# Kernel tuning notes

Measured on AMD Instinct MI355X. Metric: run time of the kernel, lower is better.

Reference implementation:

```python
import jax, jax.numpy as jnp
import numpy as np

DIM = 512
A_HEADS = 8
C_HEADS = 4
DH = 64
EPS = 1e-5


def layer_norm(x, g, b):
    mu = jnp.mean(x, axis=-1, keepdims=True)
    var = jnp.var(x, axis=-1, keepdims=True)
    return (x - mu) * jax.lax.rsqrt(var + EPS) * g + b


def setup_inputs() -> dict:
    key = jax.random.key(0)
    ks = jax.random.split(key, 8)
    inner_a = A_HEADS * DH  # 512
    inner_c = C_HEADS * DH  # 256
    s = 0.02
    return {
        "x": jax.random.normal(ks[0], (4, 192, DIM), dtype=jnp.float32),
        # Attention branch params
        "ln1_g": jnp.ones((DIM,), jnp.float32),
        "ln1_b": jnp.zeros((DIM,), jnp.float32),
        "Wqkv": jax.random.normal(ks[1], (DIM, 3 * inner_a), jnp.float32) * s,
        "Wo": jax.random.normal(ks[2], (inner_a, DIM), jnp.float32) * s,
        "bo": jnp.zeros((DIM,), jnp.float32),
        # Trittention branch params
        "ln2_g": jnp.ones((DIM,), jnp.float32),
        "ln2_b": jnp.zeros((DIM,), jnp.float32),
        "Wabcde": jax.random.normal(ks[3], (DIM, 5 * inner_c), jnp.float32) * s,
        "babcde": jnp.zeros((5 * inner_c,), jnp.float32),
        "Wp": jax.random.normal(ks[4], (inner_c, DIM), jnp.float32) * s,
        "bp": jnp.zeros((DIM,), jnp.float32),
    }


def _attention(x, ln_g, ln_b, Wqkv, Wo, bo):
    B, T, _ = x.shape
    xn = layer_norm(x, ln_g, ln_b)
    qkv = xn @ Wqkv  # [B,T,3*H*D]
    q, k, v = jnp.split(qkv, 3, axis=-1)
    def heads(t):
        return t.reshape(B, T, A_HEADS, DH).transpose(0, 2, 1, 3)  # [B,H,T,D]
    q, k, v = heads(q), heads(k), heads(v)
    scale = DH ** -0.5
    dots = jnp.einsum('bhqd,bhkd->bhqk', q, k) * scale
    attn = jax.nn.softmax(dots, axis=-1)
    out = jnp.einsum('bhqk,bhkd->bhqd', attn, v)
    out = out.transpose(0, 2, 1, 3).reshape(B, T, A_HEADS * DH)
    return out @ Wo + bo


def _trittention(x, ln_g, ln_b, Wabcde, babcde, Wp, bp):
    B, T, _ = x.shape
    xn = layer_norm(x, ln_g, ln_b)
    proj = xn @ Wabcde + babcde  # [B,T,5*H*D]
    a, b_, c, d_, e = jnp.split(proj, 5, axis=-1)
    def heads(t):
        return t.reshape(B, T, C_HEADS, DH)  # [B,T,H,D]
    a, b_, c, d_, e = heads(a), heads(b_), heads(c), heads(d_), heads(e)
    # cubic score: [B,H,S,T,Q]
    score = jnp.einsum('bshd,bthd,bqhd->bhstq', a, b_, c) / DH
    # softmax over joint (s,t) for each query q
    score = score.transpose(0, 1, 4, 2, 3).reshape(B, C_HEADS, T, T * T)
    attn = jax.nn.softmax(score, axis=-1).reshape(B, C_HEADS, T, T, T)
    z = (jnp.einsum('bhqst,bshd->bhqd', attn, d_)
         + jnp.einsum('bhqst,bthd->bhqd', attn, e))
    z = z.transpose(0, 2, 1, 3).reshape(B, T, C_HEADS * DH)
    return z @ Wp + bp


def reference(x, ln1_g, ln1_b, Wqkv, Wo, bo, ln2_g, ln2_b, Wabcde, babcde, Wp, bp):
    return (_attention(x, ln1_g, ln1_b, Wqkv, Wo, bo)
            + _trittention(x, ln2_g, ln2_b, Wabcde, babcde, Wp, bp))
```

## Files before the change

kernel.cpp:

```cpp
#include <hip/hip_runtime.h>
#include <cstdint>


#define B_   4
#define T_   192
#define DIM_ 512
#define AH   8
#define CH   4

typedef unsigned short u16;
typedef unsigned int   u32;
typedef __attribute__((ext_vector_type(8))) short short8;
typedef __attribute__((ext_vector_type(4))) float floatx4;
typedef __attribute__((ext_vector_type(4))) int intx4;
typedef __attribute__((ext_vector_type(2))) float f32x2;
typedef __attribute__((ext_vector_type(8))) _Float16 half8;
typedef __attribute__((ext_vector_type(2))) _Float16 half2v;
typedef __attribute__((ext_vector_type(2))) __fp16 fp16x2;

union Frag  { intx4 i; short8 s; };
union FragH { intx4 i; half8 h; };

__device__ __forceinline__ floatx4 mfma16(Frag a, Frag b, floatx4 c) {
    return __builtin_amdgcn_mfma_f32_16x16x32_bf16(a.s, b.s, c, 0, 0, 0);
}
__device__ __forceinline__ floatx4 mfma16h(FragH a, FragH b, floatx4 c) {
    return __builtin_amdgcn_mfma_f32_16x16x32_f16(a.h, b.h, c, 0, 0, 0);
}

__device__ __forceinline__ float fexp2(float x) {
    return __builtin_amdgcn_exp2f(x);
}

__device__ __forceinline__ float wave_reduce_sum(float v) {
#pragma unroll
    for (int off = 32; off >= 1; off >>= 1)
        v += __shfl_xor(v, off, 64);
    return v;
}

__device__ __forceinline__ u32 pack_rne(float x, float y) {
    u32 ux = __float_as_uint(x);
    u32 uy = __float_as_uint(y);
    ux += 0x7fffu + ((ux >> 16) & 1u);
    uy += 0x7fffu + ((uy >> 16) & 1u);
    return (ux >> 16) | (uy & 0xffff0000u);
}
__device__ __forceinline__ u16 bf16_rne(float x) {
    u32 u = __float_as_uint(x);
    u += 0x7fffu + ((u >> 16) & 1u);
    return (u16)(u >> 16);
}
__device__ __forceinline__ float bf16f(u16 h) { return __uint_as_float(((u32)h) << 16); }

__device__ __forceinline__ u32 pack_f16(float x, float y) {
    union { fp16x2 h; u32 u; } cv;
    cv.h = __builtin_amdgcn_cvt_pkrtz(x, y);
    return cv.u;
}
__device__ __forceinline__ u32 mul_h2(u32 a, u32 b) {
    union { u32 u; half2v h; } ua, ub, uw;
    ua.u = a; ub.u = b;
    uw.h = ua.h * ub.h;
    return uw.u;
}

__device__ __forceinline__ Frag ld_frag8(const u16* p) {
    Frag f;
    uint2 a = *(const uint2*)p;
    uint2 b = *(const uint2*)(p + 4);
    f.i = (intx4){ (int)a.x, (int)a.y, (int)b.x, (int)b.y };
    return f;
}

#define LOG2E 1.44269504088896f

__global__ __launch_bounds__(256) void prep_kernel(
    const float* __restrict__ x,
    const float* __restrict__ g1, const float* __restrict__ b1,
    const float* __restrict__ g2, const float* __restrict__ b2,
    u16* __restrict__ x1h, u16* __restrict__ x2h,
    const float* __restrict__ Wqkv, u16* __restrict__ wqh,
    const float* __restrict__ Wab,  u16* __restrict__ wah,
    const float* __restrict__ Wo,   const float* __restrict__ Wp,
    u16* __restrict__ wofh)
{
    __shared__ union { float t[64][65]; float red[4][2]; } u;
    const int tid = threadIdx.x;
    if (blockIdx.x < 768) {
        int row = blockIdx.x;
        const float2 v = ((const float2*)(x + (size_t)row * DIM_))[tid];
        float s  = v.x + v.y;
        float s2 = v.x * v.x + v.y * v.y;
        s  = wave_reduce_sum(s);
        s2 = wave_reduce_sum(s2);
        int w = tid >> 6;
        if ((tid & 63) == 0) { u.red[w][0] = s; u.red[w][1] = s2; }
        __syncthreads();
        float ts  = u.red[0][0] + u.red[1][0] + u.red[2][0] + u.red[3][0];
        float ts2 = u.red[0][1] + u.red[1][1] + u.red[2][1] + u.red[3][1];
        float mean = ts * (1.0f / DIM_);
        float var  = ts2 * (1.0f / DIM_) - mean * mean;
        float rstd = rsqrtf(var + 1e-5f);
        int c0 = tid * 2;
        float n0 = (v.x - mean) * rstd;
        float n1 = (v.y - mean) * rstd;
        float a0 = n0 * g1[c0] + b1[c0], a1 = n1 * g1[c0 + 1] + b1[c0 + 1];
        float c2 = n0 * g2[c0] + b2[c0], c3 = n1 * g2[c0 + 1] + b2[c0 + 1];
        size_t o = (size_t)row * 256 + tid;
        ((u32*)x1h)[o] = pack_rne(a0, a1);
        ((u32*)x2h)[o] = pack_rne(c2, c3);
        return;
    }
    int id = blockIdx.x - 768;
    const float* W; u16 *H; int K, N, Kout, kofs, tile;
    if (id < 192)      { W = Wqkv; H = wqh;  K = 512; N = 1536; Kout = 512; kofs = 0;   tile = id;       }
    else if (id < 352) { W = Wab;  H = wah;  K = 512; N = 1280; Kout = 512; kofs = 0;   tile = id - 192; }
    else if (id < 416) { W = Wo;   H = wofh; K = 512; N = 512;  Kout = 768; kofs = 0;   tile = id - 352; }
    else               { W = Wp;   H = wofh; K = 256; N = 512;  Kout = 768; kofs = 512; tile = id - 416; }
    int nx = N >> 6;
    int n0 = (tile % nx) * 64, k0 = (tile / nx) * 64;
    int rr = tid >> 4, c4 = (tid & 15) << 2;
#pragma unroll
    for (int p = 0; p < 4; ++p) {
        int row = rr + p * 16;
        float4 v = *(const float4*)(W + (size_t)(k0 + row) * N + n0 + c4);
        u.t[row][c4 + 0] = v.x; u.t[row][c4 + 1] = v.y;
        u.t[row][c4 + 2] = v.z; u.t[row][c4 + 3] = v.w;
    }
    __syncthreads();
#pragma unroll
    for (int p = 0; p < 4; ++p) {
        int n = rr + p * 16;
        u16 hi[4];
#pragma unroll
        for (int c = 0; c < 4; ++c)
            hi[c] = bf16_rne(u.t[c4 + c][n]);
        size_t o = (size_t)(n0 + n) * Kout + kofs + k0 + c4;
        *(uint2*)&H[o] = make_uint2((u32)hi[0] | ((u32)hi[1] << 16), (u32)hi[2] | ((u32)hi[3] << 16));
    }
}

__global__ __launch_bounds__(256) void gemm_dual(
    const u16* __restrict__ x1h, const u16* __restrict__ wqh,
    const u16* __restrict__ x2h, const u16* __restrict__ wah,
    const float* __restrict__ babcde,
    float* __restrict__ qkv, float* __restrict__ proj)
{
    __shared__ u16 As[64][68];
    __shared__ u16 Bs[64][68];
    const int tid = threadIdx.x;
    const int nb = blockIdx.x;
    const u16 *Ah, *BTh; const float* bias; float* C; int N, bn;
    if (nb < 24) { Ah = x1h; BTh = wqh; bias = nullptr; C = qkv;  N = 1536; bn = nb * 64; }
    else         { Ah = x2h; BTh = wah; bias = babcde; C = proj; N = 1280; bn = (nb - 24) * 64; }
    const int K = 512;
    const int bm = blockIdx.y * 64;
    const int lane = tid & 63, wave = tid >> 6;
    const int m16 = lane & 15, quad = lane >> 4;
    const int wm = (wave >> 1) * 32, wn = (wave & 1) * 32;
    const int r = tid >> 2, c16 = (tid & 3) * 16;

    floatx4 acc[2][2];
#pragma unroll
    for (int i = 0; i < 2; ++i)
#pragma unroll
        for (int j = 0; j < 2; ++j) acc[i][j] = (floatx4){0.f, 0.f, 0.f, 0.f};

    for (int k0 = 0; k0 < K; k0 += 64) {
        __syncthreads();
        {
            const u16* pa = Ah + (size_t)(bm + r) * K + k0 + c16;
            uint4 v0 = *(const uint4*)pa, v1 = *(const uint4*)(pa + 8);
            *(uint2*)&As[r][c16 + 0]  = make_uint2(v0.x, v0.y);
            *(uint2*)&As[r][c16 + 4]  = make_uint2(v0.z, v0.w);
            *(uint2*)&As[r][c16 + 8]  = make_uint2(v1.x, v1.y);
            *(uint2*)&As[r][c16 + 12] = make_uint2(v1.z, v1.w);
        }
        {
            const u16* pb = BTh + (size_t)(bn + r) * K + k0 + c16;
            uint4 v0 = *(const uint4*)pb, v1 = *(const uint4*)(pb + 8);
            *(uint2*)&Bs[r][c16 + 0]  = make_uint2(v0.x, v0.y);
            *(uint2*)&Bs[r][c16 + 4]  = make_uint2(v0.z, v0.w);
            *(uint2*)&Bs[r][c16 + 8]  = make_uint2(v1.x, v1.y);
            *(uint2*)&Bs[r][c16 + 12] = make_uint2(v1.z, v1.w);
        }
        __syncthreads();
#pragma unroll
        for (int ks = 0; ks < 2; ++ks) {
            const int ko = ks * 32 + quad * 8;
            Frag a0 = ld_frag8(&As[wm + m16][ko]);
            Frag a1 = ld_frag8(&As[wm + 16 + m16][ko]);
            Frag b0 = ld_frag8(&Bs[wn + m16][ko]);
            Frag b1 = ld_frag8(&Bs[wn + 16 + m16][ko]);
            acc[0][0] = mfma16(a0, b0, acc[0][0]);
            acc[0][1] = mfma16(a0, b1, acc[0][1]);
            acc[1][0] = mfma16(a1, b0, acc[1][0]);
            acc[1][1] = mfma16(a1, b1, acc[1][1]);
        }
    }
#pragma unroll
    for (int i = 0; i < 2; ++i)
#pragma unroll
        for (int rr = 0; rr < 4; ++rr) {
            int m = bm + wm + i * 16 + quad * 4 + rr;
#pragma unroll
            for (int j = 0; j < 2; ++j) {
                int n = bn + wn + j * 16 + m16;
                float v = acc[i][j][rr];
                if (bias) v += bias[n];
                C[(size_t)m * N + n] = v;
            }
        }
}

__global__ __launch_bounds__(256) void gemm_epilogue(
    const u16* __restrict__ aoh, const u16* __restrict__ zh,
    const u16* __restrict__ BTh,
    const float* __restrict__ bo, const float* __restrict__ bp,
    float* __restrict__ C)
{
    __shared__ u16 As[32][68];
    __shared__ u16 Bs[64][68];
    const int tid = threadIdx.x;
    const int bm = blockIdx.y * 32, bn = blockIdx.x * 64;
    const int lane = tid & 63, wave = tid >> 6;
    const int m16 = lane & 15, quad = lane >> 4;
    const int wm = (wave >> 1) * 16, wn = (wave & 1) * 32;
    const int ra = tid >> 3, c8 = (tid & 7) * 8;
    const int rb = tid >> 2, c16 = (tid & 3) * 16;
    const int N = 512, K = 768;

    floatx4 acc[2];
    acc[0] = (floatx4){0.f, 0.f, 0.f, 0.f};
    acc[1] = (floatx4){0.f, 0.f, 0.f, 0.f};

    for (int k0 = 0; k0 < K; k0 += 64) {
        __syncthreads();
        {
            const u16* pah = (k0 < 512)
                ? aoh + (size_t)(bm + ra) * 512 + k0 + c8
                : zh  + (size_t)(bm + ra) * 256 + (k0 - 512) + c8;
            uint4 v = *(const uint4*)pah;
            *(uint2*)&As[ra][c8 + 0] = make_uint2(v.x, v.y);
            *(uint2*)&As[ra][c8 + 4] = make_uint2(v.z, v.w);
        }
        {
            const u16* pb = BTh + (size_t)(bn + rb) * K + k0 + c16;
            uint4 v0 = *(const uint4*)pb, v1 = *(const uint4*)(pb + 8);
            *(uint2*)&Bs[rb][c16 + 0]  = make_uint2(v0.x, v0.y);
            *(uint2*)&Bs[rb][c16 + 4]  = make_uint2(v0.z, v0.w);
            *(uint2*)&Bs[rb][c16 + 8]  = make_uint2(v1.x, v1.y);
            *(uint2*)&Bs[rb][c16 + 12] = make_uint2(v1.z, v1.w);
        }
        __syncthreads();
#pragma unroll
        for (int ks = 0; ks < 2; ++ks) {
            const int ko = ks * 32 + quad * 8;
            Frag ah = ld_frag8(&As[wm + m16][ko]);
            Frag b0 = ld_frag8(&Bs[wn + m16][ko]);
            Frag b1 = ld_frag8(&Bs[wn + 16 + m16][ko]);
            acc[0] = mfma16(ah, b0, acc[0]);
            acc[1] = mfma16(ah, b1, acc[1]);
        }
    }
#pragma unroll
    for (int rr = 0; rr < 4; ++rr) {
        int m = bm + wm + quad * 4 + rr;
#pragma unroll
        for (int j = 0; j < 2; ++j) {
            int n = bn + wn + j * 16 + m16;
            C[(size_t)m * N + n] = acc[j][rr] + bo[n] + bp[n];
        }
    }
}

__global__ __launch_bounds__(256) void attn_mfma(
    const float* __restrict__ qkv, u16* __restrict__ aoh)
{
    __shared__ union { u16 Ks[192][68]; u16 P[32][196]; } KP;
    __shared__ union { u16 Vt[64][196]; struct { float m[2][16][68]; float r[2][16]; } mg; } VU;
    const int qt = blockIdx.x, h = blockIdx.y, b = blockIdx.z;
    const int tid = threadIdx.x;
    const int lane = tid & 63, wave = tid >> 6;
    const int m16 = lane & 15, quad = lane >> 4;
    const int qg = wave & 1;
    const int kh = wave >> 1;
    const size_t base = (size_t)(b * T_) * 1536 + h * 64;

    for (int i = tid; i < 192 * 16; i += 256) {
        int row = i >> 4, c4 = (i & 15) << 2;
        float4 kv = *(const float4*)(qkv + base + (size_t)row * 1536 + 512 + c4);
        *(uint2*)&KP.Ks[row][c4] = make_uint2(pack_rne(kv.x, kv.y), pack_rne(kv.z, kv.w));
        float4 vv = *(const float4*)(qkv + base + (size_t)row * 1536 + 1024 + c4);
        VU.Vt[c4 + 0][row] = bf16_rne(vv.x);
        VU.Vt[c4 + 1][row] = bf16_rne(vv.y);
        VU.Vt[c4 + 2][row] = bf16_rne(vv.z);
        VU.Vt[c4 + 3][row] = bf16_rne(vv.w);
    }

    Frag qf0, qf1;
    {
        const float s = 0.125f * LOG2E;
        const float* qp = qkv + base + (size_t)(qt * 32 + qg * 16 + m16) * 1536 + quad * 8;
        float4 u0 = *(const float4*)qp;
        float4 u1 = *(const float4*)(qp + 4);
        float4 u2 = *(const float4*)(qp + 32);
        float4 u3 = *(const float4*)(qp + 36);
        qf0.i = (intx4){ (int)pack_rne(u0.x * s, u0.y * s), (int)pack_rne(u0.z * s, u0.w * s),
                         (int)pack_rne(u1.x * s, u1.y * s), (int)pack_rne(u1.z * s, u1.w * s) };
        qf1.i = (intx4){ (int)pack_rne(u2.x * s, u2.y * s), (int)pack_rne(u2.z * s, u2.w * s),
                         (int)pack_rne(u3.x * s, u3.y * s), (int)pack_rne(u3.z * s, u3.w * s) };
    }
    __syncthreads();

    float ev[6][4];
    float rsum[4] = {0.f, 0.f, 0.f, 0.f};
#pragma unroll
    for (int tt = 0; tt < 6; ++tt) {
        const int krow = kh * 96 + tt * 16 + m16;
        Frag kb0 = ld_frag8(&KP.Ks[krow][quad * 8]);
        Frag kb1 = ld_frag8(&KP.Ks[krow][32 + quad * 8]);
        floatx4 accs = (floatx4){0.f, 0.f, 0.f, 0.f};
        accs = mfma16(qf0, kb0, accs);
        accs = mfma16(qf1, kb1, accs);
#pragma unroll
        for (int rr = 0; rr < 4; ++rr) {
            float e = fexp2(accs[rr]);
            ev[tt][rr] = e;
            rsum[rr] += e;
        }
    }
#pragma unroll
    for (int rr = 0; rr < 4; ++rr) {
        float v = rsum[rr];
        v += __shfl_xor(v, 1, 64);
        v += __shfl_xor(v, 2, 64);
        v += __shfl_xor(v, 4, 64);
        v += __shfl_xor(v, 8, 64);
        rsum[rr] = v;
    }

    __syncthreads();
#pragma unroll
    for (int tt = 0; tt < 6; ++tt)
#pragma unroll
        for (int rr = 0; rr < 4; ++rr)
            KP.P[qg * 16 + quad * 4 + rr][kh * 96 + tt * 16 + m16] = bf16_rne(ev[tt][rr]);

    floatx4 acco[4];
#pragma unroll
    for (int dt = 0; dt < 4; ++dt) acco[dt] = (floatx4){0.f, 0.f, 0.f, 0.f};
#pragma unroll
    for (int ts = 0; ts < 3; ++ts) {
        Frag pf = ld_frag8(&KP.P[qg * 16 + m16][kh * 96 + ts * 32 + quad * 8]);
#pragma unroll
        for (int dt = 0; dt < 4; ++dt) {
            Frag vf = ld_frag8(&VU.Vt[dt * 16 + m16][kh * 96 + ts * 32 + quad * 8]);
            acco[dt] = mfma16(pf, vf, acco[dt]);
        }
    }

    __syncthreads();
    if (kh == 1) {
#pragma unroll
        for (int dt = 0; dt < 4; ++dt)
#pragma unroll
            for (int rr = 0; rr < 4; ++rr)
                VU.mg.m[qg][quad * 4 + rr][dt * 16 + m16] = acco[dt][rr];
        if (m16 == 0) {
#pragma unroll
            for (int rr = 0; rr < 4; ++rr)
                VU.mg.r[qg][quad * 4 + rr] = rsum[rr];
        }
    }
    __syncthreads();
    if (kh == 0) {
        float rinv[4];
#pragma unroll
        for (int rr = 0; rr < 4; ++rr)
            rinv[rr] = 1.0f / (rsum[rr] + VU.mg.r[qg][quad * 4 + rr]);
#pragma unroll
        for (int dt = 0; dt < 4; ++dt)
#pragma unroll
            for (int rr = 0; rr < 4; ++rr) {
                float o = (acco[dt][rr] + VU.mg.m[qg][quad * 4 + rr][dt * 16 + m16]) * rinv[rr];
                size_t idx = (size_t)(b * T_ + qt * 32 + qg * 16 + quad * 4 + rr) * 512
                           + h * 64 + dt * 16 + m16;
                aoh[idx] = bf16_rne(o);
            }
    }
}

__global__ __launch_bounds__(256, 3) void tritt_score_mfma(
    const float* __restrict__ proj, float* __restrict__ rs_g, float* __restrict__ rt_g)
{
    __shared__ u32 a_lds[48 * 36];
    __shared__ u32 b_lds[48 * 36];
    __shared__ float rs_lds[48][33];
    __shared__ float rt_lds[48][33];

    const int h = blockIdx.y, b = blockIdx.z;
    const int qt = blockIdx.x >> 4;
    const int sc = (blockIdx.x >> 2) & 3;
    const int tc = blockIdx.x & 3;
    const int q0 = qt * 32, s0 = sc * 48, t0 = tc * 48;
    const int tid  = threadIdx.x;
    const int lane = tid & 63, wave = tid >> 6;
    const int m16  = lane & 15, quad = lane >> 4;
    const int bh = b * CH + h;
    const size_t rowbase = (size_t)(b * T_) * 1280 + h * 64;
    const float kA = 0.015625f * LOG2E;

    for (int i = tid; i < 48 * 32; i += 256) {
        int row = i >> 5, cp = i & 31;
        const float2 va = *(const float2*)(proj + rowbase + (size_t)(s0 + row) * 1280 + 0 + cp * 2);
        a_lds[row * 36 + cp] = pack_f16(va.x * kA, va.y * kA);
        const float2 vb = *(const float2*)(proj + rowbase + (size_t)(t0 + row) * 1280 + 256 + cp * 2);
        b_lds[row * 36 + cp] = pack_f16(vb.x, vb.y);
    }

    FragH cf[2][2];
#pragma unroll
    for (int jq = 0; jq < 2; ++jq) {
        const float* cp = proj + rowbase + (size_t)(q0 + jq * 16 + m16) * 1280 + 512 + quad * 8;
        float4 u0 = *(const float4*)(cp);
        float4 u1 = *(const float4*)(cp + 4);
        float4 u2 = *(const float4*)(cp + 32);
        float4 u3 = *(const float4*)(cp + 36);
        cf[jq][0].i = (intx4){ (int)pack_f16(u0.x, u0.y), (int)pack_f16(u0.z, u0.w),
                               (int)pack_f16(u1.x, u1.y), (int)pack_f16(u1.z, u1.w) };
        cf[jq][1].i = (intx4){ (int)pack_f16(u2.x, u2.y), (int)pack_f16(u2.z, u2.w),
                               (int)pack_f16(u3.x, u3.y), (int)pack_f16(u3.z, u3.w) };
    }
    __syncthreads();

    float rt_acc[3][4][2] = {};

    for (int si = 0; si < 12; ++si) {
        const int srow = wave * 12 + si;
        const intx4 av0 = *(const intx4*)(a_lds + srow * 36 + quad * 4);
        const intx4 av1 = *(const intx4*)(a_lds + srow * 36 + 16 + quad * 4);
        float rs_s[2] = {0.f, 0.f};
#pragma unroll
        for (int tt = 0; tt < 3; ++tt) {
            const u32* bp = b_lds + (tt * 16 + m16) * 36;
            intx4 bv0 = *(const intx4*)(bp + quad * 4);
            intx4 bv1 = *(const intx4*)(bp + 16 + quad * 4);
            FragH w0, w1;
#pragma unroll
            for (int j = 0; j < 4; ++j) {
                w0.i[j] = (int)mul_h2((u32)av0[j], (u32)bv0[j]);
                w1.i[j] = (int)mul_h2((u32)av1[j], (u32)bv1[j]);
            }
#pragma unroll
            for (int jq = 0; jq < 2; ++jq) {
                floatx4 acc = (floatx4){0.f, 0.f, 0.f, 0.f};
                acc = mfma16h(w0, cf[jq][0], acc);
                acc = mfma16h(w1, cf[jq][1], acc);
#pragma unroll
                for (int rr = 0; rr < 4; ++rr) {
                    float e = fexp2(acc[rr]);
                    rt_acc[tt][rr][jq] += e;
                    rs_s[jq] += e;
                }
            }
        }
#pragma unroll
        for (int jq = 0; jq < 2; ++jq) {
            float v = rs_s[jq];
            v += __shfl_xor(v, 16, 64);
            v += __shfl_xor(v, 32, 64);
            if (lane < 16) rs_lds[srow][jq * 16 + m16] = v;
        }
    }

    __syncthreads();
    for (int w = 0; w < 4; ++w) {
        if (wave == w) {
#pragma unroll
            for (int tt = 0; tt < 3; ++tt)
#pragma unroll
                for (int rr = 0; rr < 4; ++rr) {
                    int t = tt * 16 + quad * 4 + rr;
#pragma unroll
                    for (int jq = 0; jq < 2; ++jq) {
                        if (w == 0) rt_lds[t][jq * 16 + m16] = rt_acc[tt][rr][jq];
                        else        rt_lds[t][jq * 16 + m16] += rt_acc[tt][rr][jq];
                    }
                }
        }
        __syncthreads();
    }
    for (int i = tid; i < 32 * 48; i += 256) {
        int qq = i / 48, ss = i - qq * 48;
        rs_g[((size_t)(tc * 16 + bh) * T_ + q0 + qq) * T_ + s0 + ss] = rs_lds[ss][qq];
    }
    for (int i = tid; i < 32 * 48; i += 256) {
        int qq = i / 48, t2 = i - qq * 48;
        rt_g[((size_t)(sc * 16 + bh) * T_ + q0 + qq) * T_ + t0 + t2] = rt_lds[t2][qq];
    }
}

__global__ __launch_bounds__(256) void zgemm(
    const float* __restrict__ rs_g, const float* __restrict__ rt_g,
    const float* __restrict__ proj, u16* __restrict__ zzh)
{
    __shared__ u16 As[2][32][68];
    __shared__ u16 Bs[64][68];
    __shared__ float zred[32][9];
    __shared__ float Zl[32];
    const int mt = blockIdx.x, bh = blockIdx.y;
    const int b = bh >> 2, h = bh & 3;
    const int q0 = mt * 32;
    const int tid = threadIdx.x;
    const int lane = tid & 63, wave = tid >> 6;
    const int m16 = lane & 15, quad = lane >> 4;
    const int wm = (wave >> 1) * 16, wn = (wave & 1) * 32;
    const int ra = tid >> 3, c8 = (tid & 7) * 8;
    const int sl = tid >> 2, d4b = (tid & 3) * 4;

    float zacc = 0.f;
    floatx4 acc[2];
    acc[0] = (floatx4){0.f, 0.f, 0.f, 0.f};
    acc[1] = (floatx4){0.f, 0.f, 0.f, 0.f};

    for (int k0 = 0; k0 < 384; k0 += 64) {
        __syncthreads();
        {
            float g[8];
#pragma unroll
            for (int i = 0; i < 8; ++i) g[i] = 0.f;
            if (k0 < 192) {
#pragma unroll
                for (int tc = 0; tc < 4; ++tc) {
                    const float* p = rs_g + ((size_t)(tc * 16 + bh) * T_ + q0 + ra) * T_ + k0 + c8;
                    float4 v0 = *(const float4*)(p);
                    float4 v1 = *(const float4*)(p + 4);
                    g[0] += v0.x; g[1] += v0.y; g[2] += v0.z; g[3] += v0.w;
                    g[4] += v1.x; g[5] += v1.y; g[6] += v1.z; g[7] += v1.w;
                }
                zacc += ((g[0] + g[1]) + (g[2] + g[3])) + ((g[4] + g[5]) + (g[6] + g[7]));
            } else {
#pragma unroll
                for (int sc = 0; sc < 4; ++sc) {
                    const float* p = rt_g + ((size_t)(sc * 16 + bh) * T_ + q0 + ra) * T_ + (k0 - 192) + c8;
                    float4 v0 = *(const float4*)(p);
                    float4 v1 = *(const float4*)(p + 4);
                    g[0] += v0.x; g[1] += v0.y; g[2] += v0.z; g[3] += v0.w;
                    g[4] += v1.x; g[5] += v1.y; g[6] += v1.z; g[7] += v1.w;
                }
            }
#pragma unroll
            for (int i = 0; i < 8; ++i) {
                u16 hi = bf16_rne(g[i]);
                As[0][ra][c8 + i] = hi;
                As[1][ra][c8 + i] = bf16_rne(g[i] - bf16f(hi));
            }
        }
        {
            const int colbase = (k0 < 192 ? 768 : 1024) + h * 64;
            const int s0 = (k0 < 192 ? k0 : k0 - 192);
#pragma unroll
            for (int i = 0; i < 4; ++i) {
                int dd = d4b + i * 16;
                float4 v = *(const float4*)(proj + (size_t)(b * T_ + s0 + sl) * 1280 + colbase + dd);
                Bs[dd + 0][sl] = bf16_rne(v.x);
                Bs[dd + 1][sl] = bf16_rne(v.y);
                Bs[dd + 2][sl] = bf16_rne(v.z);
                Bs[dd + 3][sl] = bf16_rne(v.w);
            }
        }
        __syncthreads();
#pragma unroll
        for (int ks = 0; ks < 2; ++ks) {
            const int ko = ks * 32 + quad * 8;
            Frag gh = ld_frag8(&As[0][wm + m16][ko]);
            Frag gl = ld_frag8(&As[1][wm + m16][ko]);
            Frag d0 = ld_frag8(&Bs[wn + m16][ko]);
            Frag d1 = ld_frag8(&Bs[wn + 16 + m16][ko]);
            acc[0] = mfma16(gh, d0, acc[0]);
            acc[0] = mfma16(gl, d0, acc[0]);
            acc[1] = mfma16(gh, d1, acc[1]);
            acc[1] = mfma16(gl, d1, acc[1]);
        }
    }
    zred[ra][tid & 7] = zacc;
    __syncthreads();
    if (tid < 32) {
        float s = ((zred[tid][0] + zred[tid][1]) + (zred[tid][2] + zred[tid][3]))
                + ((zred[tid][4] + zred[tid][5]) + (zred[tid][6] + zred[tid][7]));
        Zl[tid] = 1.0f / s;
    }
    __syncthreads();
#pragma unroll
    for (int j = 0; j < 2; ++j)
#pragma unroll
        for (int rr = 0; rr < 4; ++rr) {
            int m = wm + quad * 4 + rr;
            int d = wn + j * 16 + m16;
            float zv = acc[j][rr] * Zl[m];
            size_t idx = (size_t)(b * T_ + q0 + m) * 256 + h * 64 + d;
            zzh[idx] = bf16_rne(zv);
        }
}

extern "C" void kernel_launch(void* const* d_in, const int* in_sizes, int n_in,
                              void* d_out, int out_size, void* d_ws, size_t ws_size,
                              hipStream_t stream)
{
    const float* x      = (const float*)d_in[0];
    const float* ln1_g  = (const float*)d_in[1];
    const float* ln1_b  = (const float*)d_in[2];
    const float* Wqkv   = (const float*)d_in[3];
    const float* Wo     = (const float*)d_in[4];
    const float* bo     = (const float*)d_in[5];
    const float* ln2_g  = (const float*)d_in[6];
    const float* ln2_b  = (const float*)d_in[7];
    const float* Wabcde = (const float*)d_in[8];
    const float* babcde = (const float*)d_in[9];
    const float* Wp     = (const float*)d_in[10];
    const float* bp     = (const float*)d_in[11];
    float* out = (float*)d_out;

    float* ws   = (float*)d_ws;
    float* proj = ws;
    u16* wofh   = (u16*)(proj + 983040);
    u16* aoh    = (u16*)(ws + 1376256);
    u16* zh     = (u16*)(ws + 1769472);
    float* rs   = ws + 1966080;
    float* rt   = rs + 2359296;
    float* qkv = rs;
    u16* x1h = (u16*)(rs + 1179648);
    u16* x2h = x1h + 393216;
    u16* wqh = (u16*)rt;
    u16* wah = wqh + 786432;

    prep_kernel<<<1216, 256, 0, stream>>>(x, ln1_g, ln1_b, ln2_g, ln2_b,
                                          x1h, x2h,
                                          Wqkv, wqh, Wabcde, wah,
                                          Wo, Wp, wofh);
    gemm_dual<<<dim3(44, 12), 256, 0, stream>>>(x1h, wqh, x2h, wah,
                                                babcde, qkv, proj);
    attn_mfma<<<dim3(6, AH, B_), 256, 0, stream>>>(qkv, aoh);
    tritt_score_mfma<<<dim3(96, CH, B_), 256, 0, stream>>>(proj, rs, rt);
    zgemm<<<dim3(6, 16), 256, 0, stream>>>(rs, rt, proj, zh);
    gemm_epilogue<<<dim3(8, 24), 256, 0, stream>>>(aoh, zh, wofh, bo, bp, out);
}
```

Before: 157.2 us.

## Reduce trittention partial row sums with atomics instead of per-chunk buffers

The score kernel now atomically adds its partial rs/rt sums into a single per-(b,h) buffer instead of writing four separate chunk buffers, and zgemm reads one buffer instead of summing four. The accumulation buffers are zeroed inside the attention kernel, which runs earlier, to avoid an extra memset launch. The goal is less global write and read traffic. In exchange it adds float atomic contention, makes the summation order nondeterministic, and reshuffles the workspace aliasing so x1h/x2h now share memory with the zeroed buffers.

```diff
diff --git a/kernel.cpp b/kernel.cpp
--- a/kernel.cpp
+++ b/kernel.cpp
@@ -276,12 +276,18 @@
 }
 
 __global__ __launch_bounds__(256) void attn_mfma(
-    const float* __restrict__ qkv, u16* __restrict__ aoh)
+    const float* __restrict__ qkv, u16* __restrict__ aoh, float* __restrict__ zero_base)
 {
     __shared__ union { u16 Ks[192][68]; u16 P[32][196]; } KP;
     __shared__ union { u16 Vt[64][196]; struct { float m[2][16][68]; float r[2][16]; } mg; } VU;
     const int qt = blockIdx.x, h = blockIdx.y, b = blockIdx.z;
     const int tid = threadIdx.x;
+    {
+        float4* z4 = (float4*)zero_base;
+        const float4 z = make_float4(0.f, 0.f, 0.f, 0.f);
+        int gid = ((b * AH + h) * 6 + qt) * 256 + tid;
+        for (int i = gid; i < 294912; i += 49152) z4[i] = z;
+    }
     const int lane = tid & 63, wave = tid >> 6;
     const int m16 = lane & 15, quad = lane >> 4;
     const int qg = wave & 1;
@@ -393,7 +399,7 @@
 }
 
 __global__ __launch_bounds__(256, 3) void tritt_score_mfma(
-    const float* __restrict__ proj, float* __restrict__ rs_g, float* __restrict__ rt_g)
+    const float* __restrict__ proj, float* __restrict__ rs1, float* __restrict__ rt1)
 {
     __shared__ u32 a_lds[48 * 36];
     __shared__ u32 b_lds[48 * 36];
@@ -494,16 +500,16 @@
     }
     for (int i = tid; i < 32 * 48; i += 256) {
         int qq = i / 48, ss = i - qq * 48;
-        rs_g[((size_t)(tc * 16 + bh) * T_ + q0 + qq) * T_ + s0 + ss] = rs_lds[ss][qq];
+        unsafeAtomicAdd(&rs1[((size_t)bh * T_ + q0 + qq) * T_ + s0 + ss], rs_lds[ss][qq]);
     }
     for (int i = tid; i < 32 * 48; i += 256) {
         int qq = i / 48, t2 = i - qq * 48;
-        rt_g[((size_t)(sc * 16 + bh) * T_ + q0 + qq) * T_ + t0 + t2] = rt_lds[t2][qq];
+        unsafeAtomicAdd(&rt1[((size_t)bh * T_ + q0 + qq) * T_ + t0 + t2], rt_lds[t2][qq]);
     }
 }
 
 __global__ __launch_bounds__(256) void zgemm(
-    const float* __restrict__ rs_g, const float* __restrict__ rt_g,
+    const float* __restrict__ rs1, const float* __restrict__ rt1,
     const float* __restrict__ proj, u16* __restrict__ zzh)
 {
     __shared__ u16 As[2][32][68];
@@ -529,27 +535,19 @@
         __syncthreads();
         {
             float g[8];
-#pragma unroll
-            for (int i = 0; i < 8; ++i) g[i] = 0.f;
             if (k0 < 192) {
-#pragma unroll
-                for (int tc = 0; tc < 4; ++tc) {
-                    const float* p = rs_g + ((size_t)(tc * 16 + bh) * T_ + q0 + ra) * T_ + k0 + c8;
-                    float4 v0 = *(const float4*)(p);
-                    float4 v1 = *(const float4*)(p + 4);
-                    g[0] += v0.x; g[1] += v0.y; g[2] += v0.z; g[3] += v0.w;
-                    g[4] += v1.x; g[5] += v1.y; g[6] += v1.z; g[7] += v1.w;
-                }
+                const float* p = rs1 + ((size_t)bh * T_ + q0 + ra) * T_ + k0 + c8;
+                float4 v0 = *(const float4*)(p);
+                float4 v1 = *(const float4*)(p + 4);
+                g[0] = v0.x; g[1] = v0.y; g[2] = v0.z; g[3] = v0.w;
+                g[4] = v1.x; g[5] = v1.y; g[6] = v1.z; g[7] = v1.w;
                 zacc += ((g[0] + g[1]) + (g[2] + g[3])) + ((g[4] + g[5]) + (g[6] + g[7]));
             } else {
-#pragma unroll
-                for (int sc = 0; sc < 4; ++sc) {
-                    const float* p = rt_g + ((size_t)(sc * 16 + bh) * T_ + q0 + ra) * T_ + (k0 - 192) + c8;
-                    float4 v0 = *(const float4*)(p);
-                    float4 v1 = *(const float4*)(p + 4);
-                    g[0] += v0.x; g[1] += v0.y; g[2] += v0.z; g[3] += v0.w;
-                    g[4] += v1.x; g[5] += v1.y; g[6] += v1.z; g[7] += v1.w;
-                }
+                const float* p = rt1 + ((size_t)bh * T_ + q0 + ra) * T_ + (k0 - 192) + c8;
+                float4 v0 = *(const float4*)(p);
+                float4 v1 = *(const float4*)(p + 4);
+                g[0] = v0.x; g[1] = v0.y; g[2] = v0.z; g[3] = v0.w;
+                g[4] = v1.x; g[5] = v1.y; g[6] = v1.z; g[7] = v1.w;
             }
 #pragma unroll
             for (int i = 0; i < 8; ++i) {
@@ -628,12 +626,12 @@
     u16* wofh   = (u16*)(proj + 983040);
     u16* aoh    = (u16*)(ws + 1376256);
     u16* zh     = (u16*)(ws + 1769472);
-    float* rs   = ws + 1966080;
-    float* rt   = rs + 2359296;
-    float* qkv = rs;
-    u16* x1h = (u16*)(rs + 1179648);
+    float* qkv  = ws + 1966080;
+    float* rs1  = ws + 1966080 + 1179648;
+    float* rt1  = rs1 + 589824;
+    u16* x1h = (u16*)rs1;
     u16* x2h = x1h + 393216;
-    u16* wqh = (u16*)rt;
+    u16* wqh = (u16*)(rt1 + 589824);
     u16* wah = wqh + 786432;
 
     prep_kernel<<<1216, 256, 0, stream>>>(x, ln1_g, ln1_b, ln2_g, ln2_b,
@@ -642,8 +640,8 @@
                                           Wo, Wp, wofh);
     gemm_dual<<<dim3(44, 12), 256, 0, stream>>>(x1h, wqh, x2h, wah,
                                                 babcde, qkv, proj);
-    attn_mfma<<<dim3(6, AH, B_), 256, 0, stream>>>(qkv, aoh);
-    tritt_score_mfma<<<dim3(96, CH, B_), 256, 0, stream>>>(proj, rs, rt);
-    zgemm<<<dim3(6, 16), 256, 0, stream>>>(rs, rt, proj, zh);
+    attn_mfma<<<dim3(6, AH, B_), 256, 0, stream>>>(qkv, aoh, rs1);
+    tritt_score_mfma<<<dim3(96, CH, B_), 256, 0, stream>>>(proj, rs1, rt1);
+    zgemm<<<dim3(6, 16), 256, 0, stream>>>(rs1, rt1, proj, zh);
     gemm_epilogue<<<dim3(8, 24), 256, 0, stream>>>(aoh, zh, wofh, bo, bp, out);
 }
```

New measurement: 158.2 us. Within noise of the previous version (+0.6%).
